# Optimization experiments

Measured on AMD Instinct MI355X. Metric: run time of the kernel, lower is better.

## Reference

```python
import jax, jax.numpy as jnp
import numpy as np

GROUPS = 4
KLD_SCALE = 10.0
COMMIT_COST = 0.25


def setup_inputs() -> dict:
    key = jax.random.key(0)
    k1, k2, k3, k4 = jax.random.split(key, 4)
    B, H, C = 8, 4096, 512
    n_embed, d = 512, C // GROUPS
    return {
        "z": jax.random.normal(k1, (B, H, C), dtype=jnp.float32),
        "embed_w": jax.random.normal(k2, (n_embed, d), dtype=jnp.float32),
        "proj_w": jax.random.normal(k3, (C, C), dtype=jnp.float32) * (1.0 / np.sqrt(C)),
        "proj_b": jax.random.normal(k4, (C,), dtype=jnp.float32) * 0.01,
    }


def reference(z, embed_w, proj_w, proj_b):
    B, H, C = z.shape
    d = C // GROUPS
    sg = jax.lax.stop_gradient
    # split channels into groups -> [B, H*groups, d]
    z_e = z.reshape(B, H * GROUPS, d)
    flat = z_e.reshape(-1, d)  # [N, d]
    dist = ((flat ** 2).sum(1, keepdims=True)
            - 2.0 * flat @ embed_w.T
            + (embed_w ** 2).sum(1)[None, :])  # [N, n_embed]
    ind = jnp.argmin(dist, axis=1).reshape(B, H * GROUPS)  # (-dist).max == dist.min
    z_q = embed_w[ind]  # [B, H*groups, d]
    diff = KLD_SCALE * (COMMIT_COST * jnp.mean((sg(z_q) - z_e) ** 2)
                        + jnp.mean((z_q - sg(z_e)) ** 2))
    # straight-through estimator
    z_q = z_e + sg(z_q - z_e)
    z_q = z_q.reshape(B, H, C)
    out = z_q @ proj_w.T + proj_b
    return out, diff, ind
```

## Files before the change

kernel.cpp:

```cpp
#include <hip/hip_runtime.h>

constexpr int D         = 128;
constexpr int NE        = 512;
constexpr int NROWS     = 131072;
constexpr int CC        = 512;
constexpr int OUT_ELEMS = 16777216;


using half8  = __attribute__((ext_vector_type(8))) _Float16;
using f32x16 = __attribute__((ext_vector_type(16))) float;

#define F16_MINNORM 6.103515625e-05f

#define AS_STRIDE 68
#define AS_S4 17

__launch_bounds__(256, 4)
__global__ void prep_kernel(const float* __restrict__ embed,
                            const float* __restrict__ projw,
                            unsigned short* __restrict__ esw,
                            float* __restrict__ entab,
                            float* __restrict__ ws_diff,
                            float* __restrict__ P) {
    __shared__ float As[64 * AS_STRIDE];
    __shared__ float Bs[64 * AS_STRIDE];
    const int tid = threadIdx.x;

    if (blockIdx.x >= 256) {
        const int chunk = blockIdx.x - 256;
        const int cl = tid >> 3;
        const int seg = tid & 7;
        const float* src = embed + (size_t)(chunk * 32 + cl) * D + seg * 16;
        unsigned short* cb = esw + (size_t)chunk * 8192;

        float ss = 0.f;
#pragma unroll
        for (int g2 = 0; g2 < 2; g2++) {
            float4 a = ((const float4*)src)[g2 * 2 + 0];
            float4 b = ((const float4*)src)[g2 * 2 + 1];
            float v[8] = {a.x, a.y, a.z, a.w, b.x, b.y, b.z, b.w};
            half8 t1, t2;
#pragma unroll
            for (int i = 0; i < 8; i++) {
                ss += v[i] * v[i];
                float m2 = -2.0f * v[i];
                float m2c = (__builtin_fabsf(m2) < F16_MINNORM) ? 0.0f : m2;
                _Float16 h = (_Float16)m2c;
                float r = m2 - (float)h;
                t1[i] = h;
                t2[i] = (_Float16)(r * 2048.0f);
            }
            const int idx = seg * 512 + g2 * 256 + cl * 8;
            *(half8*)(cb + idx) = t1;
            *(half8*)(cb + 4096 + idx) = t2;
        }
        ss += __shfl_down(ss, 4, 8);
        ss += __shfl_down(ss, 2, 8);
        ss += __shfl_down(ss, 1, 8);
        if (seg == 0) entab[chunk * 32 + cl] = ss;
        if (chunk == 0 && tid == 0) ws_diff[0] = 0.0f;
        return;
    }

    const int b = blockIdx.x;
    const int cbase = (b & 7) * 64;
    const int jbase = ((b >> 3) & 7) * 64;
    const int g = b >> 6;
    const int tx = tid & 15, ty = tid >> 4;
    const int r = tid >> 2, seg = tid & 3;

    float acc[4][4];
#pragma unroll
    for (int i = 0; i < 4; i++)
#pragma unroll
        for (int j = 0; j < 4; j++) acc[i][j] = 0.f;

    for (int kb = 0; kb < D; kb += 64) {
        const float4* asrc = (const float4*)(embed + (size_t)(jbase + r) * D + kb + seg * 16);
        const float4* bsrc = (const float4*)(projw + (size_t)(cbase + r) * CC + g * D + kb + seg * 16);
        float4* adst = (float4*)&As[r * AS_STRIDE + seg * 16];
        float4* bdst = (float4*)&Bs[r * AS_STRIDE + seg * 16];
#pragma unroll
        for (int q = 0; q < 4; q++) { adst[q] = asrc[q]; bdst[q] = bsrc[q]; }
        __syncthreads();

        const float4* as4 = (const float4*)As;
        const float4* bs4 = (const float4*)Bs;
#pragma unroll 4
        for (int kk = 0; kk < 16; kk++) {
            float4 a[4], bb[4];
#pragma unroll
            for (int i = 0; i < 4; i++) a[i] = as4[(ty + 16 * i) * AS_S4 + kk];
#pragma unroll
            for (int j = 0; j < 4; j++) bb[j] = bs4[(tx + 16 * j) * AS_S4 + kk];
#pragma unroll
            for (int i = 0; i < 4; i++)
#pragma unroll
                for (int j = 0; j < 4; j++)
                    acc[i][j] += a[i].x * bb[j].x + a[i].y * bb[j].y +
                                 a[i].z * bb[j].z + a[i].w * bb[j].w;
        }
        __syncthreads();
    }
#pragma unroll
    for (int j = 0; j < 4; j++) {
#pragma unroll
        for (int i = 0; i < 4; i++)
            P[(size_t)g * 262144 + (size_t)(jbase + ty + 16 * i) * CC + cbase + tx + 16 * j] =
                acc[i][j];
    }
}

__global__ __launch_bounds__(256, 3)
void argmin_fused_kernel(const float* __restrict__ z,
                         const unsigned short* __restrict__ esw,
                         const float* __restrict__ entab,
                         const float* __restrict__ P,
                         const float* __restrict__ projb,
                         float* __restrict__ ws_diff,
                         float* __restrict__ ind_f,
                         float* __restrict__ out) {
    __shared__ __align__(16) unsigned char ebuf[3 * 16384];
    __shared__ __align__(16) float entab_s[512];
    const int tid = threadIdx.x;
    const int lane = tid & 63;
    const int wave = tid >> 6;
    const int h5 = lane >> 5, l5 = lane & 31;
    const int rb = blockIdx.x * 128 + wave * 32;

    auto stage = [&](int c, int b) {
        const unsigned char* s = (const unsigned char*)esw + (size_t)c * 16384 +
                                 wave * 4096 + lane * 16;
        unsigned char* d = &ebuf[b * 16384 + wave * 4096];
#pragma unroll
        for (int it = 0; it < 4; it++)
            __builtin_amdgcn_global_load_lds(
                (const __attribute__((address_space(1))) unsigned int*)(s + it * 1024),
                (__attribute__((address_space(3))) unsigned int*)(d + it * 1024),
                16, 0, 0);
    };

    if (tid < 128)
        __builtin_amdgcn_global_load_lds(
            (const __attribute__((address_space(1))) unsigned int*)(entab + tid * 4),
            (__attribute__((address_space(3))) unsigned int*)(entab_s + tid * 4),
            16, 0, 0);
    stage(0, 0);
    stage(1, 1);

    half8 x1[8], x2[8];
    float xn = 0.f;
    {
        const float* zr = z + (size_t)(rb + l5) * D + h5 * 8;
#pragma unroll
        for (int kk = 0; kk < 8; kk++) {
            float4 a = *(const float4*)(zr + kk * 16);
            float4 b = *(const float4*)(zr + kk * 16 + 4);
            float v[8] = {a.x, a.y, a.z, a.w, b.x, b.y, b.z, b.w};
            half8 t1, t2;
#pragma unroll
            for (int i = 0; i < 8; i++) {
                xn += v[i] * v[i];
                float vc = (__builtin_fabsf(v[i]) < F16_MINNORM) ? 0.0f : v[i];
                _Float16 h = (_Float16)vc;
                float r = v[i] - (float)h;
                t1[i] = h;
                t2[i] = (_Float16)(r * 2048.0f);
            }
            x1[kk] = t1; x2[kk] = t2;
        }
    }

    float minv = 3.0e38f;
    int   mini = 0;

    int bs = 0;
    int ts = 2;
#pragma unroll 1
    for (int c = 0; c < 16; c++) {
        if (c < 15) { asm volatile("s_waitcnt vmcnt(4)" ::: "memory"); }
        else        { asm volatile("s_waitcnt vmcnt(0)" ::: "memory"); }
        __builtin_amdgcn_s_barrier();
        __builtin_amdgcn_sched_barrier(0);
        if (c < 14) stage(c + 2, ts);

        const unsigned char* ldsb = &ebuf[bs * 16384];

        f32x16 accA = (f32x16)(0.0f), accB = (f32x16)(0.0f);
#pragma unroll
        for (int kk = 0; kk < 8; kk++) {
            const int fo = kk * 1024 + h5 * 512 + l5 * 16;
            half8 e1 = *(const half8*)(ldsb + fo);
            half8 e2 = *(const half8*)(ldsb + 8192 + fo);
            accA = __builtin_amdgcn_mfma_f32_32x32x16_f16(e1, x1[kk], accA, 0, 0, 0);
            accB = __builtin_amdgcn_mfma_f32_32x32x16_f16(e1, x2[kk], accB, 0, 0, 0);
            accB = __builtin_amdgcn_mfma_f32_32x32x16_f16(e2, x1[kk], accB, 0, 0, 0);
        }

        float4 enr[4];
#pragma unroll
        for (int u = 0; u < 4; u++)
            enr[u] = *(const float4*)&entab_s[c * 32 + h5 * 4 + u * 8];

        const int cb2 = c * 32 + h5 * 4;
#pragma unroll
        for (int r = 0; r < 16; r++) {
            const float en = ((const float*)&enr[r >> 2])[r & 3];
            const int cand = cb2 + (r & 3) + 8 * (r >> 2);
            float d0 = fmaf(accB[r], 4.8828125e-4f, accA[r]) + en;
            if (d0 < minv) { minv = d0; mini = cand; }
        }
        bs = (bs == 2) ? 0 : bs + 1;
        ts = (ts == 2) ? 0 : ts + 1;
    }

    {
        float ov = __shfl_xor(minv, 32);
        int oi = __shfl_xor(mini, 32);
        if (ov < minv || (ov == minv && oi < mini)) { minv = ov; mini = oi; }
    }
    if (lane < 32) ind_f[rb + l5] = (float)mini;

    const int ob = rb >> 2;
    const float4* P4  = (const float4*)P;
    const float4* pb4 = (const float4*)projb;
    float4* out4 = (float4*)out;
    const float4 bias0 = pb4[lane];
    const float4 bias1 = pb4[64 + lane];
#pragma unroll 2
    for (int r = 0; r < 8; r++) {
        const int ig0 = __shfl(mini, r * 4 + 0);
        const int ig1 = __shfl(mini, r * 4 + 1);
        const int ig2 = __shfl(mini, r * 4 + 2);
        const int ig3 = __shfl(mini, r * 4 + 3);
#pragma unroll
        for (int p = 0; p < 2; p++) {
            const int c4 = p * 64 + lane;
            float4 acc = p ? bias1 : bias0;
            float4 a0 = P4[(size_t)ig0 * 128 + c4];
            float4 a1 = P4[ 65536 + (size_t)ig1 * 128 + c4];
            float4 a2 = P4[131072 + (size_t)ig2 * 128 + c4];
            float4 a3 = P4[196608 + (size_t)ig3 * 128 + c4];
            acc.x += a0.x + a1.x + a2.x + a3.x;
            acc.y += a0.y + a1.y + a2.y + a3.y;
            acc.z += a0.z + a1.z + a2.z + a3.z;
            acc.w += a0.w + a1.w + a2.w + a3.w;
            out4[(size_t)(ob + r) * 128 + c4] = acc;
        }
    }

    float xfull = xn + __shfl_xor(xn, 32);
    float v = (lane < 32) ? (xfull + minv) : 0.0f;
#pragma unroll
    for (int off = 32; off; off >>= 1) v += __shfl_down(v, off);
    if (lane == 0) atomicAdd(ws_diff, v);
}

__global__ void finalize_kernel(const float* __restrict__ ws_diff,
                                float* __restrict__ diff_out) {
    diff_out[0] = 12.5f * ws_diff[0] * (1.0f / 16777216.0f);
}

extern "C" void kernel_launch(void* const* d_in, const int* in_sizes, int n_in,
                              void* d_out, int out_size, void* d_ws, size_t ws_size,
                              hipStream_t stream) {
    const float* z     = (const float*)d_in[0];
    const float* embed = (const float*)d_in[1];
    const float* projw = (const float*)d_in[2];
    const float* projb = (const float*)d_in[3];

    float* out      = (float*)d_out;
    float* diff_out = out + OUT_ELEMS;
    float* ind_f    = out + OUT_ELEMS + 1;

    char* wsb = (char*)d_ws;
    float* ws_diff = (float*)wsb;
    float* entab = (float*)(wsb + 1024);
    unsigned short* esw = (unsigned short*)(wsb + 4096);
    float* P = (float*)(wsb + 266240);

    prep_kernel<<<272, 256, 0, stream>>>(embed, projw, esw, entab, ws_diff, P);
    argmin_fused_kernel<<<NROWS / 128, 256, 0, stream>>>(z, esw, entab, P, projb,
                                                         ws_diff, ind_f, out);
    finalize_kernel<<<1, 1, 0, stream>>>(ws_diff, diff_out);
}
```

Baseline: 216.0 us.

## Process two row tiles per wave in argmin and use MFMA for P precompute

After: 235.0 us. 8.8% more time.

```diff
diff --git a/kernel.cpp b/kernel.cpp
--- a/kernel.cpp
+++ b/kernel.cpp
@@ -12,8 +12,18 @@
 
 #define F16_MINNORM 6.103515625e-05f
 
-#define AS_STRIDE 68
-#define AS_S4 17
+__device__ __forceinline__ void split8(float4 a, float4 b,
+                                       half8& t1, half8& t2) {
+    float v[8] = {a.x, a.y, a.z, a.w, b.x, b.y, b.z, b.w};
+#pragma unroll
+    for (int i = 0; i < 8; i++) {
+        float vc = (__builtin_fabsf(v[i]) < F16_MINNORM) ? 0.0f : v[i];
+        _Float16 h = (_Float16)vc;
+        float r = v[i] - (float)h;
+        t1[i] = h;
+        t2[i] = (_Float16)(r * 2048.0f);
+    }
+}
 
 __launch_bounds__(256, 4)
 __global__ void prep_kernel(const float* __restrict__ embed,
@@ -22,12 +32,10 @@
                             float* __restrict__ entab,
                             float* __restrict__ ws_diff,
                             float* __restrict__ P) {
-    __shared__ float As[64 * AS_STRIDE];
-    __shared__ float Bs[64 * AS_STRIDE];
     const int tid = threadIdx.x;
 
-    if (blockIdx.x >= 256) {
-        const int chunk = blockIdx.x - 256;
+    if (blockIdx.x >= 64) {
+        const int chunk = blockIdx.x - 64;
         const int cl = tid >> 3;
         const int seg = tid & 7;
         const float* src = embed + (size_t)(chunk * 32 + cl) * D + seg * 16;
@@ -62,56 +70,55 @@
         return;
     }
 
-    const int b = blockIdx.x;
-    const int cbase = (b & 7) * 64;
-    const int jbase = ((b >> 3) & 7) * 64;
-    const int g = b >> 6;
-    const int tx = tid & 15, ty = tid >> 4;
-    const int r = tid >> 2, seg = tid & 3;
-
-    float acc[4][4];
-#pragma unroll
-    for (int i = 0; i < 4; i++)
-#pragma unroll
-        for (int j = 0; j < 4; j++) acc[i][j] = 0.f;
-
-    for (int kb = 0; kb < D; kb += 64) {
-        const float4* asrc = (const float4*)(embed + (size_t)(jbase + r) * D + kb + seg * 16);
-        const float4* bsrc = (const float4*)(projw + (size_t)(cbase + r) * CC + g * D + kb + seg * 16);
-        float4* adst = (float4*)&As[r * AS_STRIDE + seg * 16];
-        float4* bdst = (float4*)&Bs[r * AS_STRIDE + seg * 16];
-#pragma unroll
-        for (int q = 0; q < 4; q++) { adst[q] = asrc[q]; bdst[q] = bsrc[q]; }
-        __syncthreads();
-
-        const float4* as4 = (const float4*)As;
-        const float4* bs4 = (const float4*)Bs;
-#pragma unroll 4
-        for (int kk = 0; kk < 16; kk++) {
-            float4 a[4], bb[4];
-#pragma unroll
-            for (int i = 0; i < 4; i++) a[i] = as4[(ty + 16 * i) * AS_S4 + kk];
-#pragma unroll
-            for (int j = 0; j < 4; j++) bb[j] = bs4[(tx + 16 * j) * AS_S4 + kk];
-#pragma unroll
-            for (int i = 0; i < 4; i++)
-#pragma unroll
-                for (int j = 0; j < 4; j++)
-                    acc[i][j] += a[i].x * bb[j].x + a[i].y * bb[j].y +
-                                 a[i].z * bb[j].z + a[i].w * bb[j].w;
-        }
-        __syncthreads();
-    }
-#pragma unroll
-    for (int j = 0; j < 4; j++) {
-#pragma unroll
-        for (int i = 0; i < 4; i++)
-            P[(size_t)g * 262144 + (size_t)(jbase + ty + 16 * i) * CC + cbase + tx + 16 * j] =
-                acc[i][j];
-    }
-}
-
-__global__ __launch_bounds__(256, 3)
+    const int lane = tid & 63;
+    const int wave = tid >> 6;
+    const int h5 = lane >> 5, l5 = lane & 31;
+    const int job  = blockIdx.x * 4 + wave;
+    const int g    = job >> 6;
+    const int cblk = (job >> 2) & 15;
+    const int quad = job & 3;
+
+    half8 wh[8], wl[8];
+    {
+        const float* wr = projw + (size_t)(cblk * 32 + l5) * CC + g * D + h5 * 8;
+#pragma unroll
+        for (int kk = 0; kk < 8; kk++) {
+            float4 a = *(const float4*)(wr + kk * 16);
+            float4 b = *(const float4*)(wr + kk * 16 + 4);
+            split8(a, b, wh[kk], wl[kk]);
+        }
+    }
+
+#pragma unroll 1
+    for (int q = 0; q < 4; q++) {
+        const int ch = quad * 4 + q;
+        half8 eh[8], el[8];
+        {
+            const float* er = embed + (size_t)(ch * 32 + l5) * D + h5 * 8;
+#pragma unroll
+            for (int kk = 0; kk < 8; kk++) {
+                float4 a = *(const float4*)(er + kk * 16);
+                float4 b = *(const float4*)(er + kk * 16 + 4);
+                split8(a, b, eh[kk], el[kk]);
+            }
+        }
+        f32x16 accA = (f32x16)(0.0f), accB = (f32x16)(0.0f);
+#pragma unroll
+        for (int kk = 0; kk < 8; kk++) {
+            accA = __builtin_amdgcn_mfma_f32_32x32x16_f16(eh[kk], wh[kk], accA, 0, 0, 0);
+            accB = __builtin_amdgcn_mfma_f32_32x32x16_f16(eh[kk], wl[kk], accB, 0, 0, 0);
+            accB = __builtin_amdgcn_mfma_f32_32x32x16_f16(el[kk], wh[kk], accB, 0, 0, 0);
+        }
+#pragma unroll
+        for (int r = 0; r < 16; r++) {
+            const int jl = (r & 3) + 8 * (r >> 2) + 4 * h5;
+            P[(size_t)g * 262144 + (size_t)(ch * 32 + jl) * CC + cblk * 32 + l5] =
+                fmaf(accB[r], 4.8828125e-4f, accA[r]);
+        }
+    }
+}
+
+__global__ __launch_bounds__(256, 2)
 void argmin_fused_kernel(const float* __restrict__ z,
                          const unsigned short* __restrict__ esw,
                          const float* __restrict__ entab,
@@ -126,7 +133,8 @@
     const int lane = tid & 63;
     const int wave = tid >> 6;
     const int h5 = lane >> 5, l5 = lane & 31;
-    const int rb = blockIdx.x * 128 + wave * 32;
+    const int rb0 = blockIdx.x * 256 + wave * 32;
+    const int rb1 = rb0 + 128;
 
     auto stage = [&](int c, int b) {
         const unsigned char* s = (const unsigned char*)esw + (size_t)c * 16384 +
@@ -148,31 +156,31 @@
     stage(0, 0);
     stage(1, 1);
 
-    half8 x1[8], x2[8];
-    float xn = 0.f;
+    half8 x1a[8], x2a[8], x1b[8], x2b[8];
+    float xna = 0.f, xnb = 0.f;
     {
-        const float* zr = z + (size_t)(rb + l5) * D + h5 * 8;
+        const float* zr = z + (size_t)(rb0 + l5) * D + h5 * 8;
 #pragma unroll
         for (int kk = 0; kk < 8; kk++) {
             float4 a = *(const float4*)(zr + kk * 16);
             float4 b = *(const float4*)(zr + kk * 16 + 4);
-            float v[8] = {a.x, a.y, a.z, a.w, b.x, b.y, b.z, b.w};
-            half8 t1, t2;
-#pragma unroll
-            for (int i = 0; i < 8; i++) {
-                xn += v[i] * v[i];
-                float vc = (__builtin_fabsf(v[i]) < F16_MINNORM) ? 0.0f : v[i];
-                _Float16 h = (_Float16)vc;
-                float r = v[i] - (float)h;
-                t1[i] = h;
-                t2[i] = (_Float16)(r * 2048.0f);
-            }
-            x1[kk] = t1; x2[kk] = t2;
-        }
-    }
-
-    float minv = 3.0e38f;
-    int   mini = 0;
+            xna += a.x*a.x + a.y*a.y + a.z*a.z + a.w*a.w +
+                   b.x*b.x + b.y*b.y + b.z*b.z + b.w*b.w;
+            split8(a, b, x1a[kk], x2a[kk]);
+        }
+        const float* zr2 = z + (size_t)(rb1 + l5) * D + h5 * 8;
+#pragma unroll
+        for (int kk = 0; kk < 8; kk++) {
+            float4 a = *(const float4*)(zr2 + kk * 16);
+            float4 b = *(const float4*)(zr2 + kk * 16 + 4);
+            xnb += a.x*a.x + a.y*a.y + a.z*a.z + a.w*a.w +
+                   b.x*b.x + b.y*b.y + b.z*b.z + b.w*b.w;
+            split8(a, b, x1b[kk], x2b[kk]);
+        }
+    }
+
+    float minva = 3.0e38f, minvb = 3.0e38f;
+    int   minia = 0,       minib = 0;
 
     int bs = 0;
     int ts = 2;
@@ -186,15 +194,19 @@
 
         const unsigned char* ldsb = &ebuf[bs * 16384];
 
-        f32x16 accA = (f32x16)(0.0f), accB = (f32x16)(0.0f);
+        f32x16 accA0 = (f32x16)(0.0f), accB0 = (f32x16)(0.0f);
+        f32x16 accA1 = (f32x16)(0.0f), accB1 = (f32x16)(0.0f);
 #pragma unroll
         for (int kk = 0; kk < 8; kk++) {
             const int fo = kk * 1024 + h5 * 512 + l5 * 16;
             half8 e1 = *(const half8*)(ldsb + fo);
             half8 e2 = *(const half8*)(ldsb + 8192 + fo);
-            accA = __builtin_amdgcn_mfma_f32_32x32x16_f16(e1, x1[kk], accA, 0, 0, 0);
-            accB = __builtin_amdgcn_mfma_f32_32x32x16_f16(e1, x2[kk], accB, 0, 0, 0);
-            accB = __builtin_amdgcn_mfma_f32_32x32x16_f16(e2, x1[kk], accB, 0, 0, 0);
+            accA0 = __builtin_amdgcn_mfma_f32_32x32x16_f16(e1, x1a[kk], accA0, 0, 0, 0);
+            accB0 = __builtin_amdgcn_mfma_f32_32x32x16_f16(e1, x2a[kk], accB0, 0, 0, 0);
+            accB0 = __builtin_amdgcn_mfma_f32_32x32x16_f16(e2, x1a[kk], accB0, 0, 0, 0);
+            accA1 = __builtin_amdgcn_mfma_f32_32x32x16_f16(e1, x1b[kk], accA1, 0, 0, 0);
+            accB1 = __builtin_amdgcn_mfma_f32_32x32x16_f16(e1, x2b[kk], accB1, 0, 0, 0);
+            accB1 = __builtin_amdgcn_mfma_f32_32x32x16_f16(e2, x1b[kk], accB1, 0, 0, 0);
         }
 
         float4 enr[4];
@@ -207,21 +219,29 @@
         for (int r = 0; r < 16; r++) {
             const float en = ((const float*)&enr[r >> 2])[r & 3];
             const int cand = cb2 + (r & 3) + 8 * (r >> 2);
-            float d0 = fmaf(accB[r], 4.8828125e-4f, accA[r]) + en;
-            if (d0 < minv) { minv = d0; mini = cand; }
+            float d0 = fmaf(accB0[r], 4.8828125e-4f, accA0[r]) + en;
+            if (d0 < minva) { minva = d0; minia = cand; }
+            float d1 = fmaf(accB1[r], 4.8828125e-4f, accA1[r]) + en;
+            if (d1 < minvb) { minvb = d1; minib = cand; }
         }
         bs = (bs == 2) ? 0 : bs + 1;
         ts = (ts == 2) ? 0 : ts + 1;
     }
 
     {
-        float ov = __shfl_xor(minv, 32);
-        int oi = __shfl_xor(mini, 32);
-        if (ov < minv || (ov == minv && oi < mini)) { minv = ov; mini = oi; }
-    }
-    if (lane < 32) ind_f[rb + l5] = (float)mini;
-
-    const int ob = rb >> 2;
+        float ov = __shfl_xor(minva, 32);
+        int oi = __shfl_xor(minia, 32);
+        if (ov < minva || (ov == minva && oi < minia)) { minva = ov; minia = oi; }
+        float ov1 = __shfl_xor(minvb, 32);
+        int oi1 = __shfl_xor(minib, 32);
+        if (ov1 < minvb || (ov1 == minvb && oi1 < minib)) { minvb = ov1; minib = oi1; }
+    }
+    if (lane < 32) {
+        ind_f[rb0 + l5] = (float)minia;
+        ind_f[rb1 + l5] = (float)minib;
+    }
+
+    const int ob0 = rb0 >> 2;
     const float4* P4  = (const float4*)P;
     const float4* pb4 = (const float4*)projb;
     float4* out4 = (float4*)out;
@@ -229,10 +249,10 @@
     const float4 bias1 = pb4[64 + lane];
 #pragma unroll 2
     for (int r = 0; r < 8; r++) {
-        const int ig0 = __shfl(mini, r * 4 + 0);
-        const int ig1 = __shfl(mini, r * 4 + 1);
-        const int ig2 = __shfl(mini, r * 4 + 2);
-        const int ig3 = __shfl(mini, r * 4 + 3);
+        const int ig0 = __shfl(minia, r * 4 + 0);
+        const int ig1 = __shfl(minia, r * 4 + 1);
+        const int ig2 = __shfl(minia, r * 4 + 2);
+        const int ig3 = __shfl(minia, r * 4 + 3);
 #pragma unroll
         for (int p = 0; p < 2; p++) {
             const int c4 = p * 64 + lane;
@@ -245,12 +265,34 @@
             acc.y += a0.y + a1.y + a2.y + a3.y;
             acc.z += a0.z + a1.z + a2.z + a3.z;
             acc.w += a0.w + a1.w + a2.w + a3.w;
-            out4[(size_t)(ob + r) * 128 + c4] = acc;
-        }
-    }
-
-    float xfull = xn + __shfl_xor(xn, 32);
-    float v = (lane < 32) ? (xfull + minv) : 0.0f;
+            out4[(size_t)(ob0 + r) * 128 + c4] = acc;
+        }
+    }
+#pragma unroll 2
+    for (int r = 0; r < 8; r++) {
+        const int ig0 = __shfl(minib, r * 4 + 0);
+        const int ig1 = __shfl(minib, r * 4 + 1);
+        const int ig2 = __shfl(minib, r * 4 + 2);
+        const int ig3 = __shfl(minib, r * 4 + 3);
+#pragma unroll
+        for (int p = 0; p < 2; p++) {
+            const int c4 = p * 64 + lane;
+            float4 acc = p ? bias1 : bias0;
+            float4 a0 = P4[(size_t)ig0 * 128 + c4];
+            float4 a1 = P4[ 65536 + (size_t)ig1 * 128 + c4];
+            float4 a2 = P4[131072 + (size_t)ig2 * 128 + c4];
+            float4 a3 = P4[196608 + (size_t)ig3 * 128 + c4];
+            acc.x += a0.x + a1.x + a2.x + a3.x;
+            acc.y += a0.y + a1.y + a2.y + a3.y;
+            acc.z += a0.z + a1.z + a2.z + a3.z;
+            acc.w += a0.w + a1.w + a2.w + a3.w;
+            out4[(size_t)(ob0 + 32 + r) * 128 + c4] = acc;
+        }
+    }
+
+    float xfa = xna + __shfl_xor(xna, 32);
+    float xfb = xnb + __shfl_xor(xnb, 32);
+    float v = (lane < 32) ? (xfa + minva + xfb + minvb) : 0.0f;
 #pragma unroll
     for (int off = 32; off; off >>= 1) v += __shfl_down(v, off);
     if (lane == 0) atomicAdd(ws_diff, v);
@@ -279,8 +321,8 @@
     unsigned short* esw = (unsigned short*)(wsb + 4096);
     float* P = (float*)(wsb + 266240);
 
-    prep_kernel<<<272, 256, 0, stream>>>(embed, projw, esw, entab, ws_diff, P);
-    argmin_fused_kernel<<<NROWS / 128, 256, 0, stream>>>(z, esw, entab, P, projb,
+    prep_kernel<<<80, 256, 0, stream>>>(embed, projw, esw, entab, ws_diff, P);
+    argmin_fused_kernel<<<NROWS / 256, 256, 0, stream>>>(z, esw, entab, P, projb,
                                                          ws_diff, ind_f, out);
     finalize_kernel<<<1, 1, 0, stream>>>(ws_diff, diff_out);
 }
```

## Compute projected codebook table with split-f16 MFMA and add nontemporal z/out access

Applied to the files above, without the earlier changes.

After: 221.7 us. 2.7% more time.

```diff
diff --git a/kernel.cpp b/kernel.cpp
--- a/kernel.cpp
+++ b/kernel.cpp
@@ -9,25 +9,34 @@
 
 using half8  = __attribute__((ext_vector_type(8))) _Float16;
 using f32x16 = __attribute__((ext_vector_type(16))) float;
+using f32x4  = __attribute__((ext_vector_type(4))) float;
 
 #define F16_MINNORM 6.103515625e-05f
 
-#define AS_STRIDE 68
-#define AS_S4 17
-
-__launch_bounds__(256, 4)
+__device__ __forceinline__ void split8v(f32x4 a, f32x4 b,
+                                        half8& t1, half8& t2) {
+    float v[8] = {a[0], a[1], a[2], a[3], b[0], b[1], b[2], b[3]};
+#pragma unroll
+    for (int i = 0; i < 8; i++) {
+        float vc = (__builtin_fabsf(v[i]) < F16_MINNORM) ? 0.0f : v[i];
+        _Float16 h = (_Float16)vc;
+        float r = v[i] - (float)h;
+        t1[i] = h;
+        t2[i] = (_Float16)(r * 2048.0f);
+    }
+}
+
+__launch_bounds__(256, 1)
 __global__ void prep_kernel(const float* __restrict__ embed,
                             const float* __restrict__ projw,
                             unsigned short* __restrict__ esw,
                             float* __restrict__ entab,
                             float* __restrict__ ws_diff,
                             float* __restrict__ P) {
-    __shared__ float As[64 * AS_STRIDE];
-    __shared__ float Bs[64 * AS_STRIDE];
     const int tid = threadIdx.x;
 
-    if (blockIdx.x >= 256) {
-        const int chunk = blockIdx.x - 256;
+    if (blockIdx.x >= 64) {
+        const int chunk = blockIdx.x - 64;
         const int cl = tid >> 3;
         const int seg = tid & 7;
         const float* src = embed + (size_t)(chunk * 32 + cl) * D + seg * 16;
@@ -36,9 +45,9 @@
         float ss = 0.f;
 #pragma unroll
         for (int g2 = 0; g2 < 2; g2++) {
-            float4 a = ((const float4*)src)[g2 * 2 + 0];
-            float4 b = ((const float4*)src)[g2 * 2 + 1];
-            float v[8] = {a.x, a.y, a.z, a.w, b.x, b.y, b.z, b.w};
+            f32x4 a = ((const f32x4*)src)[g2 * 2 + 0];
+            f32x4 b = ((const f32x4*)src)[g2 * 2 + 1];
+            float v[8] = {a[0], a[1], a[2], a[3], b[0], b[1], b[2], b[3]};
             half8 t1, t2;
 #pragma unroll
             for (int i = 0; i < 8; i++) {
@@ -62,52 +71,51 @@
         return;
     }
 
-    const int b = blockIdx.x;
-    const int cbase = (b & 7) * 64;
-    const int jbase = ((b >> 3) & 7) * 64;
-    const int g = b >> 6;
-    const int tx = tid & 15, ty = tid >> 4;
-    const int r = tid >> 2, seg = tid & 3;
-
-    float acc[4][4];
-#pragma unroll
-    for (int i = 0; i < 4; i++)
-#pragma unroll
-        for (int j = 0; j < 4; j++) acc[i][j] = 0.f;
-
-    for (int kb = 0; kb < D; kb += 64) {
-        const float4* asrc = (const float4*)(embed + (size_t)(jbase + r) * D + kb + seg * 16);
-        const float4* bsrc = (const float4*)(projw + (size_t)(cbase + r) * CC + g * D + kb + seg * 16);
-        float4* adst = (float4*)&As[r * AS_STRIDE + seg * 16];
-        float4* bdst = (float4*)&Bs[r * AS_STRIDE + seg * 16];
-#pragma unroll
-        for (int q = 0; q < 4; q++) { adst[q] = asrc[q]; bdst[q] = bsrc[q]; }
-        __syncthreads();
-
-        const float4* as4 = (const float4*)As;
-        const float4* bs4 = (const float4*)Bs;
-#pragma unroll 4
-        for (int kk = 0; kk < 16; kk++) {
-            float4 a[4], bb[4];
-#pragma unroll
-            for (int i = 0; i < 4; i++) a[i] = as4[(ty + 16 * i) * AS_S4 + kk];
-#pragma unroll
-            for (int j = 0; j < 4; j++) bb[j] = bs4[(tx + 16 * j) * AS_S4 + kk];
-#pragma unroll
-            for (int i = 0; i < 4; i++)
-#pragma unroll
-                for (int j = 0; j < 4; j++)
-                    acc[i][j] += a[i].x * bb[j].x + a[i].y * bb[j].y +
-                                 a[i].z * bb[j].z + a[i].w * bb[j].w;
-        }
-        __syncthreads();
-    }
-#pragma unroll
-    for (int j = 0; j < 4; j++) {
-#pragma unroll
-        for (int i = 0; i < 4; i++)
-            P[(size_t)g * 262144 + (size_t)(jbase + ty + 16 * i) * CC + cbase + tx + 16 * j] =
-                acc[i][j];
+    const int lane = tid & 63;
+    const int wave = tid >> 6;
+    const int h5 = lane >> 5, l5 = lane & 31;
+    const int job  = blockIdx.x * 4 + wave;
+    const int g    = job >> 6;
+    const int cblk = (job >> 2) & 15;
+    const int quad = job & 3;
+
+    half8 wh[8], wl[8];
+    {
+        const float* wr = projw + (size_t)(cblk * 32 + l5) * CC + g * D + h5 * 8;
+#pragma unroll
+        for (int kk = 0; kk < 8; kk++) {
+            f32x4 a = *(const f32x4*)(wr + kk * 16);
+            f32x4 b = *(const f32x4*)(wr + kk * 16 + 4);
+            split8v(a, b, wh[kk], wl[kk]);
+        }
+    }
+
+#pragma unroll 1
+    for (int q = 0; q < 4; q++) {
+        const int ch = quad * 4 + q;
+        half8 eh[8], el[8];
+        {
+            const float* er = embed + (size_t)(ch * 32 + l5) * D + h5 * 8;
+#pragma unroll
+            for (int kk = 0; kk < 8; kk++) {
+                f32x4 a = *(const f32x4*)(er + kk * 16);
+                f32x4 b = *(const f32x4*)(er + kk * 16 + 4);
+                split8v(a, b, eh[kk], el[kk]);
+            }
+        }
+        f32x16 accA = (f32x16)(0.0f), accB = (f32x16)(0.0f);
+#pragma unroll
+        for (int kk = 0; kk < 8; kk++) {
+            accA = __builtin_amdgcn_mfma_f32_32x32x16_f16(eh[kk], wh[kk], accA, 0, 0, 0);
+            accB = __builtin_amdgcn_mfma_f32_32x32x16_f16(eh[kk], wl[kk], accB, 0, 0, 0);
+            accB = __builtin_amdgcn_mfma_f32_32x32x16_f16(el[kk], wh[kk], accB, 0, 0, 0);
+        }
+#pragma unroll
+        for (int r = 0; r < 16; r++) {
+            const int jl = (r & 3) + 8 * (r >> 2) + 4 * h5;
+            P[(size_t)g * 262144 + (size_t)(ch * 32 + jl) * CC + cblk * 32 + l5] =
+                fmaf(accB[r], 4.8828125e-4f, accA[r]);
+        }
     }
 }
 
@@ -151,23 +159,14 @@
     half8 x1[8], x2[8];
     float xn = 0.f;
     {
-        const float* zr = z + (size_t)(rb + l5) * D + h5 * 8;
-#pragma unroll
-        for (int kk = 0; kk < 8; kk++) {
-            float4 a = *(const float4*)(zr + kk * 16);
-            float4 b = *(const float4*)(zr + kk * 16 + 4);
-            float v[8] = {a.x, a.y, a.z, a.w, b.x, b.y, b.z, b.w};
-            half8 t1, t2;
-#pragma unroll
-            for (int i = 0; i < 8; i++) {
-                xn += v[i] * v[i];
-                float vc = (__builtin_fabsf(v[i]) < F16_MINNORM) ? 0.0f : v[i];
-                _Float16 h = (_Float16)vc;
-                float r = v[i] - (float)h;
-                t1[i] = h;
-                t2[i] = (_Float16)(r * 2048.0f);
-            }
-            x1[kk] = t1; x2[kk] = t2;
+        const f32x4* zr = (const f32x4*)(z + (size_t)(rb + l5) * D + h5 * 8);
+#pragma unroll
+        for (int kk = 0; kk < 8; kk++) {
+            f32x4 a = __builtin_nontemporal_load(zr + kk * 4);
+            f32x4 b = __builtin_nontemporal_load(zr + kk * 4 + 1);
+            xn += a[0]*a[0] + a[1]*a[1] + a[2]*a[2] + a[3]*a[3] +
+                  b[0]*b[0] + b[1]*b[1] + b[2]*b[2] + b[3]*b[3];
+            split8v(a, b, x1[kk], x2[kk]);
         }
     }
 
@@ -187,6 +186,7 @@
         const unsigned char* ldsb = &ebuf[bs * 16384];
 
         f32x16 accA = (f32x16)(0.0f), accB = (f32x16)(0.0f);
+        __builtin_amdgcn_s_setprio(1);
 #pragma unroll
         for (int kk = 0; kk < 8; kk++) {
             const int fo = kk * 1024 + h5 * 512 + l5 * 16;
@@ -196,16 +196,17 @@
             accB = __builtin_amdgcn_mfma_f32_32x32x16_f16(e1, x2[kk], accB, 0, 0, 0);
             accB = __builtin_amdgcn_mfma_f32_32x32x16_f16(e2, x1[kk], accB, 0, 0, 0);
         }
-
-        float4 enr[4];
+        __builtin_amdgcn_s_setprio(0);
+
+        f32x4 enr[4];
 #pragma unroll
         for (int u = 0; u < 4; u++)
-            enr[u] = *(const float4*)&entab_s[c * 32 + h5 * 4 + u * 8];
+            enr[u] = *(const f32x4*)&entab_s[c * 32 + h5 * 4 + u * 8];
 
         const int cb2 = c * 32 + h5 * 4;
 #pragma unroll
         for (int r = 0; r < 16; r++) {
-            const float en = ((const float*)&enr[r >> 2])[r & 3];
+            const float en = enr[r >> 2][r & 3];
             const int cand = cb2 + (r & 3) + 8 * (r >> 2);
             float d0 = fmaf(accB[r], 4.8828125e-4f, accA[r]) + en;
             if (d0 < minv) { minv = d0; mini = cand; }
@@ -222,11 +223,11 @@
     if (lane < 32) ind_f[rb + l5] = (float)mini;
 
     const int ob = rb >> 2;
-    const float4* P4  = (const float4*)P;
-    const float4* pb4 = (const float4*)projb;
-    float4* out4 = (float4*)out;
-    const float4 bias0 = pb4[lane];
-    const float4 bias1 = pb4[64 + lane];
+    const f32x4* P4  = (const f32x4*)P;
+    const f32x4* pb4 = (const f32x4*)projb;
+    f32x4* out4 = (f32x4*)out;
+    const f32x4 bias0 = pb4[lane];
+    const f32x4 bias1 = pb4[64 + lane];
 #pragma unroll 2
     for (int r = 0; r < 8; r++) {
         const int ig0 = __shfl(mini, r * 4 + 0);
@@ -236,16 +237,13 @@
 #pragma unroll
         for (int p = 0; p < 2; p++) {
             const int c4 = p * 64 + lane;
-            float4 acc = p ? bias1 : bias0;
-            float4 a0 = P4[(size_t)ig0 * 128 + c4];
-            float4 a1 = P4[ 65536 + (size_t)ig1 * 128 + c4];
-            float4 a2 = P4[131072 + (size_t)ig2 * 128 + c4];
-            float4 a3 = P4[196608 + (size_t)ig3 * 128 + c4];
-            acc.x += a0.x + a1.x + a2.x + a3.x;
-            acc.y += a0.y + a1.y + a2.y + a3.y;
-            acc.z += a0.z + a1.z + a2.z + a3.z;
-            acc.w += a0.w + a1.w + a2.w + a3.w;
-            out4[(size_t)(ob + r) * 128 + c4] = acc;
+            f32x4 acc = p ? bias1 : bias0;
+            f32x4 a0 = P4[(size_t)ig0 * 128 + c4];
+            f32x4 a1 = P4[ 65536 + (size_t)ig1 * 128 + c4];
+            f32x4 a2 = P4[131072 + (size_t)ig2 * 128 + c4];
+            f32x4 a3 = P4[196608 + (size_t)ig3 * 128 + c4];
+            acc += a0 + a1 + a2 + a3;
+            __builtin_nontemporal_store(acc, &out4[(size_t)(ob + r) * 128 + c4]);
         }
     }
 
@@ -279,7 +277,7 @@
     unsigned short* esw = (unsigned short*)(wsb + 4096);
     float* P = (float*)(wsb + 266240);
 
-    prep_kernel<<<272, 256, 0, stream>>>(embed, projw, esw, entab, ws_diff, P);
+    prep_kernel<<<80, 256, 0, stream>>>(embed, projw, esw, entab, ws_diff, P);
     argmin_fused_kernel<<<NROWS / 128, 256, 0, stream>>>(z, esw, entab, P, projb,
                                                          ws_diff, ind_f, out);
     finalize_kernel<<<1, 1, 0, stream>>>(ws_diff, diff_out);
```
